# Kernel optimization log

Measured on AMD Instinct MI355X. Metric: run time of the kernel, lower is better.

## Reference

```python
import jax, jax.numpy as jnp
import numpy as np

S, T, B = 1024, 64, 8
KEY_DIM, QUERY_DIM, HIDDEN = 512, 512, 256


def setup_inputs() -> dict:
    key = jax.random.key(0)
    ks = jax.random.split(key, 8)
    inp = {
        "key": jax.random.normal(ks[0], (S, B, KEY_DIM), dtype=jnp.float32),
        "query": jax.random.normal(ks[1], (T, B, QUERY_DIM), dtype=jnp.float32),
        # torch nn.Linear params, stored as (in, out) for x @ W
        "Wk": jax.random.normal(ks[2], (KEY_DIM, HIDDEN), dtype=jnp.float32) * (1.0 / np.sqrt(KEY_DIM)),
        "bk": jax.random.normal(ks[3], (HIDDEN,), dtype=jnp.float32) * 0.01,
        "Wq": jax.random.normal(ks[4], (QUERY_DIM, HIDDEN), dtype=jnp.float32) * (1.0 / np.sqrt(QUERY_DIM)),
        "bq": jax.random.normal(ks[5], (HIDDEN,), dtype=jnp.float32) * 0.01,
        "v": jax.random.normal(ks[6], (HIDDEN,), dtype=jnp.float32),
    }
    return inp


def reference(key, query, Wk, bk, Wq, bq, v):
    # key: (S, B, Dk), query: (T, B, Dq)
    key_proj = key @ Wk + bk          # (S, B, H)
    query_proj = query @ Wq + bq      # (T, B, H)
    # broadcast add: (T,1,B,H) + (1,S,B,H) -> (T,S,B,H)
    energy = jnp.tanh(query_proj[:, None, :, :] + key_proj[None, :, :, :])
    scores = jnp.einsum('tsbh,h->tsb', energy, v)  # (T, S, B)
    attn = jax.nn.softmax(scores, axis=1)          # softmax over key positions S
    return jnp.transpose(attn, (2, 0, 1))          # (B, T, S)
```

## Files before the change

kernel.cpp:

```cpp
#include <hip/hip_runtime.h>

#define S_DIM 1024
#define T_DIM 64
#define B_DIM 8
#define K_DIM 512
#define H_DIM 256

typedef _Float16 f16;
typedef __attribute__((ext_vector_type(4))) _Float16 f16x4;
typedef __attribute__((ext_vector_type(8))) _Float16 f16x8;
typedef __attribute__((ext_vector_type(4))) float f32x4;

__device__ __forceinline__ float fast_rcp(float x) { return __builtin_amdgcn_rcpf(x); }

__device__ __forceinline__ void gload16(const void* g, void* l) {
    __builtin_amdgcn_global_load_lds(
        (const __attribute__((address_space(1))) unsigned int*)g,
        (__attribute__((address_space(3))) unsigned int*)l, 16, 0, 0);
}

__global__ __launch_bounds__(256) void wconv_kernel(
    const float* __restrict__ Wk, const float* __restrict__ Wq,
    f16* __restrict__ WTk, f16* __restrict__ WTq)
{
    __shared__ float tile[64][65];
    const int idx = blockIdx.x;
    const float* W = (idx & 32) ? Wq : Wk;
    f16* WT = (idx & 32) ? WTq : WTk;
    const int t32 = idx & 31;
    const int k0 = (t32 >> 2) * 64, n0 = (t32 & 3) * 64;
    const int c = threadIdx.x & 63, r0 = threadIdx.x >> 6;
#pragma unroll
    for (int i = 0; i < 16; ++i) {
        int r = r0 + i * 4;
        tile[r][c] = W[(size_t)(k0 + r) * H_DIM + n0 + c];
    }
    __syncthreads();
#pragma unroll
    for (int i = 0; i < 16; ++i) {
        int r = r0 + i * 4;
        WT[(size_t)(n0 + r) * K_DIM + k0 + c] = (f16)tile[c][r];
    }
}

__global__ __launch_bounds__(256, 4) void proj_gemm_all(
    const float* __restrict__ key, const f16* __restrict__ WTk,
    const float* __restrict__ bk, float* __restrict__ ktT,
    const float* __restrict__ query, const f16* __restrict__ WTq,
    const float* __restrict__ bq, float* __restrict__ tq2)
{
    __shared__ __align__(16) char smem[2][16384];
    const int tid = threadIdx.x;
    const int lane = tid & 63, wid = tid >> 6;
    const int widu = __builtin_amdgcn_readfirstlane(wid);
    const int wm = (wid >> 1) * 16, wn = (wid & 1) * 32;

    const int bid0 = blockIdx.x;
    const int bid = (bid0 & 7) * 136 + (bid0 >> 3);
    const bool isQ = bid >= 1024;
    const int lb = isQ ? bid - 1024 : bid;
    const size_t m0 = (size_t)(lb >> 2) * 32;
    const int n0 = (lb & 3) * 64;
    const float* A    = isQ ? query : key;
    const f16* BT     = isQ ? WTq : WTk;
    const float* bias = isQ ? bq : bk;

    const int o0 = tid << 4;
    const int o1 = o0 + 4096;
    const int row0 = o0 >> 7, kb0 = (o0 & 127) ^ ((row0 & 7) << 4);
    const int row1 = o1 >> 7, kb1 = (o1 & 127) ^ ((row1 & 7) << 4);
    const char* b_t = (const char*)(BT + (size_t)n0 * K_DIM);

    auto GLOADB = [&](int buf, int t) {
        const int kb = t * 128;
        char* d0 = &smem[buf][8192 + widu * 1024];
        gload16(b_t + (size_t)row0 * 1024 + kb + kb0, d0);
        gload16(b_t + (size_t)row1 * 1024 + kb + kb1, d0 + 4096);
    };

    const float* a_base = A + m0 * K_DIM;
    float4 areg[2];
    auto ALOAD = [&](int t) {
#pragma unroll
        for (int j = 0; j < 2; ++j) {
            const int fidx = j * 256 + tid;
            const int r = fidx >> 4, c16 = fidx & 15;
            areg[j] = *(const float4*)&a_base[(size_t)r * K_DIM + t * 64 + c16 * 4];
        }
    };
    auto AWRITE = [&](int buf) {
#pragma unroll
        for (int j = 0; j < 2; ++j) {
            const int fidx = j * 256 + tid;
            const int r = fidx >> 4, c16 = fidx & 15;
            const int byt = r * 128 + ((c16 * 8) ^ ((r & 7) << 4));
            f16 h0 = (f16)areg[j].x, h1 = (f16)areg[j].y, h2 = (f16)areg[j].z, h3 = (f16)areg[j].w;
            f16x4 hi = {h0, h1, h2, h3};
            f16x4 lo = {(f16)(areg[j].x - (float)h0), (f16)(areg[j].y - (float)h1),
                        (f16)(areg[j].z - (float)h2), (f16)(areg[j].w - (float)h3)};
            *(f16x4*)&smem[buf][byt] = hi;
            *(f16x4*)&smem[buf][4096 + byt] = lo;
        }
    };

    f32x4 acc[2] = {};
    const int fr = lane & 15, fgb = (lane >> 4) << 4;

    auto COMPUTE = [&](int buf) {
#pragma unroll
        for (int kk = 0; kk < 2; ++kk) {
            const int kbyte = kk * 64 + fgb;
            const int arow = wm + fr;
            const int abyt = (arow << 7) + (kbyte ^ ((arow & 7) << 4));
            f16x8 ah = *(const f16x8*)&smem[buf][abyt];
            f16x8 al = *(const f16x8*)&smem[buf][4096 + abyt];
            const int brow0 = wn + fr, brow1 = wn + 16 + fr;
            f16x8 b0 = *(const f16x8*)&smem[buf][8192 + (brow0 << 7) + (kbyte ^ ((brow0 & 7) << 4))];
            f16x8 b1 = *(const f16x8*)&smem[buf][8192 + (brow1 << 7) + (kbyte ^ ((brow1 & 7) << 4))];
            acc[0] = __builtin_amdgcn_mfma_f32_16x16x32_f16(ah, b0, acc[0], 0, 0, 0);
            acc[1] = __builtin_amdgcn_mfma_f32_16x16x32_f16(ah, b1, acc[1], 0, 0, 0);
            acc[0] = __builtin_amdgcn_mfma_f32_16x16x32_f16(al, b0, acc[0], 0, 0, 0);
            acc[1] = __builtin_amdgcn_mfma_f32_16x16x32_f16(al, b1, acc[1], 0, 0, 0);
        }
    };

    ALOAD(0);
    GLOADB(0, 0);
    AWRITE(0);
    __syncthreads();

    int buf = 0;
#pragma unroll 1
    for (int t = 0; t < 8; ++t) {
        if (t < 7) {
            ALOAD(t + 1);
            GLOADB(buf ^ 1, t + 1);
        }
        COMPUTE(buf);
        if (t < 7) {
            AWRITE(buf ^ 1);
            __syncthreads();
        }
        buf ^= 1;
    }

    const int crow = (lane >> 4) * 4, ccol = lane & 15;
    if (isQ) {
#pragma unroll
        for (int g = 0; g < 2; ++g) {
            int col = n0 + wn + g * 16 + ccol;
            float bv = bias[col];
#pragma unroll
            for (int r = 0; r < 4; ++r) {
                size_t row = m0 + wm + crow + r;
                float val = __expf(2.0f * (acc[g][r] + bv));
                tq2[((size_t)(row & 7) * T_DIM + (row >> 3)) * H_DIM + col] = val;
            }
        }
    } else {
        float* lt = (float*)&smem[0][0];
#pragma unroll
        for (int g = 0; g < 2; ++g) {
            int lcol = wn + g * 16 + ccol;
            float bv = bias[n0 + lcol];
#pragma unroll
            for (int r = 0; r < 4; ++r) {
                int lrow = wm + crow + r;
                lt[lrow * 64 + lcol] = __expf(2.0f * (acc[g][r] + bv));
            }
        }
        __syncthreads();
        const int sbase = (int)(m0 >> 3);
        const int n0q = n0 >> 2;
#pragma unroll
        for (int p = 0; p < 2; ++p) {
            int c = p * 256 + tid;
            int s_off = c & 3, h4 = (c >> 2) & 15, b2 = c >> 6;
            float4 o = *(const float4*)&lt[(s_off * 8 + b2) * 64 + h4 * 4];
            size_t f4idx = ((size_t)b2 * 64 + n0q + h4) * S_DIM + sbase + s_off;
            *(float4*)&ktT[f4idx * 4] = o;
        }
    }
}

__global__ __launch_bounds__(1024) void scores_softmax_kernel(
    const float* __restrict__ ktT, const float* __restrict__ tq2,
    const float* __restrict__ v, float* __restrict__ out)
{
    __shared__ float redm[2][16], reds[2][16];
    const int tid = threadIdx.x, lane = tid & 63;
    const int wid = __builtin_amdgcn_readfirstlane(tid >> 6);
    const int bid = blockIdx.x;
    const int b = bid & 7;
    const int t0 = (bid >> 3) * 2;
    const int s = tid;

    const float4* kb4 = (const float4*)ktT + (size_t)b * 64 * S_DIM + s;
    const float* q0p = tq2 + ((size_t)b * T_DIM + t0) * H_DIM;
    const float* q1p = q0p + H_DIM;

    float a0 = 0.f, a1 = 0.f;
#pragma unroll 8
    for (int h4 = 0; h4 < H_DIM / 4; ++h4) {
        float4 k4 = kb4[(size_t)h4 * S_DIM];
        float4 vv = *(const float4*)&v[h4 * 4];
        float4 q0 = *(const float4*)&q0p[h4 * 4];
        float4 q1 = *(const float4*)&q1p[h4 * 4];
        float A, B;
        A = fmaf(q0.x, k4.x, 1.0f); B = fmaf(q0.y, k4.y, 1.0f);
        a0 = fmaf(fmaf(vv.x, B, vv.y * A), fast_rcp(A * B), a0);
        A = fmaf(q0.z, k4.z, 1.0f); B = fmaf(q0.w, k4.w, 1.0f);
        a0 = fmaf(fmaf(vv.z, B, vv.w * A), fast_rcp(A * B), a0);
        A = fmaf(q1.x, k4.x, 1.0f); B = fmaf(q1.y, k4.y, 1.0f);
        a1 = fmaf(fmaf(vv.x, B, vv.y * A), fast_rcp(A * B), a1);
        A = fmaf(q1.z, k4.z, 1.0f); B = fmaf(q1.w, k4.w, 1.0f);
        a1 = fmaf(fmaf(vv.z, B, vv.w * A), fast_rcp(A * B), a1);
    }
    a0 *= -2.0f;
    a1 *= -2.0f;

    float m0 = a0, m1 = a1;
#pragma unroll
    for (int mm = 32; mm >= 1; mm >>= 1) {
        m0 = fmaxf(m0, __shfl_xor(m0, mm, 64));
        m1 = fmaxf(m1, __shfl_xor(m1, mm, 64));
    }
    if (lane == 0) { redm[0][wid] = m0; redm[1][wid] = m1; }
    __syncthreads();
    m0 = redm[0][0]; m1 = redm[1][0];
#pragma unroll
    for (int i = 1; i < 16; ++i) {
        m0 = fmaxf(m0, redm[0][i]);
        m1 = fmaxf(m1, redm[1][i]);
    }

    float e0 = __expf(a0 - m0), e1 = __expf(a1 - m1);
    float s0 = e0, s1 = e1;
#pragma unroll
    for (int mm = 32; mm >= 1; mm >>= 1) {
        s0 += __shfl_xor(s0, mm, 64);
        s1 += __shfl_xor(s1, mm, 64);
    }
    if (lane == 0) { reds[0][wid] = s0; reds[1][wid] = s1; }
    __syncthreads();
    s0 = 0.f; s1 = 0.f;
#pragma unroll
    for (int i = 0; i < 16; ++i) { s0 += reds[0][i]; s1 += reds[1][i]; }

    float* o = out + ((size_t)b * T_DIM + t0) * S_DIM + s;
    o[0]     = e0 * fast_rcp(s0);
    o[S_DIM] = e1 * fast_rcp(s1);
}

extern "C" void kernel_launch(void* const* d_in, const int* in_sizes, int n_in,
                              void* d_out, int out_size, void* d_ws, size_t ws_size,
                              hipStream_t stream)
{
    const float* key   = (const float*)d_in[0];
    const float* query = (const float*)d_in[1];
    const float* Wk    = (const float*)d_in[2];
    const float* bk    = (const float*)d_in[3];
    const float* Wq    = (const float*)d_in[4];
    const float* bq    = (const float*)d_in[5];
    const float* v     = (const float*)d_in[6];
    float* out = (float*)d_out;

    float* ktT    = (float*)d_ws;
    float* tq2    = ktT + (size_t)B_DIM * H_DIM * S_DIM;
    f16* WTk = (f16*)(tq2 + (size_t)B_DIM * T_DIM * H_DIM);
    f16* WTq = WTk + (size_t)H_DIM * K_DIM;

    wconv_kernel<<<64, 256, 0, stream>>>(Wk, Wq, WTk, WTq);
    proj_gemm_all<<<1088, 256, 0, stream>>>(key, WTk, bk, ktT, query, WTq, bq, tq2);
    scores_softmax_kernel<<<256, 1024, 0, stream>>>(ktT, tq2, v, out);
}
```

Before: 44.13 us.

## Double projection GEMM M-tile to 64 rows, halving block count

The projection GEMM tile grows from 32x64 to 64x64 per block. Each wave now computes a 32x32 sub-tile with four accumulators, so every B-fragment load from LDS feeds twice as many MFMAs. The grid shrinks from 1088 to 544 blocks and the launch bound drops to 3 blocks per CU. The LDS staging for the ktT transpose is re-laid out with a padded stride of 68. The cost is more registers and LDS per block and fewer blocks to spread across CUs, which may reduce latency hiding.

New measurement: 43.09 us. 2.4% less time.

```diff
diff --git a/kernel.cpp b/kernel.cpp
--- a/kernel.cpp
+++ b/kernel.cpp
@@ -43,29 +43,29 @@
     }
 }
 
-__global__ __launch_bounds__(256, 4) void proj_gemm_all(
+__global__ __launch_bounds__(256, 3) void proj_gemm_all(
     const float* __restrict__ key, const f16* __restrict__ WTk,
     const float* __restrict__ bk, float* __restrict__ ktT,
     const float* __restrict__ query, const f16* __restrict__ WTq,
     const float* __restrict__ bq, float* __restrict__ tq2)
 {
-    __shared__ __align__(16) char smem[2][16384];
+    __shared__ __align__(16) char smem[2][3][8192];
     const int tid = threadIdx.x;
     const int lane = tid & 63, wid = tid >> 6;
     const int widu = __builtin_amdgcn_readfirstlane(wid);
-    const int wm = (wid >> 1) * 16, wn = (wid & 1) * 32;
+    const int wm = (wid >> 1) * 32, wn = (wid & 1) * 32;
 
     const int bid0 = blockIdx.x;
-    const int bid = (bid0 & 7) * 136 + (bid0 >> 3);
-    const bool isQ = bid >= 1024;
-    const int lb = isQ ? bid - 1024 : bid;
-    const size_t m0 = (size_t)(lb >> 2) * 32;
+    const int bid = (bid0 & 7) * 68 + (bid0 >> 3);
+    const bool isQ = bid >= 512;
+    const int lb = isQ ? bid - 512 : bid;
+    const size_t m0 = (size_t)(lb >> 2) * 64;
     const int n0 = (lb & 3) * 64;
     const float* A    = isQ ? query : key;
     const f16* BT     = isQ ? WTq : WTk;
     const float* bias = isQ ? bq : bk;
 
-    const int o0 = tid << 4;
+    const int o0 = wid * 1024 + (lane << 4);
     const int o1 = o0 + 4096;
     const int row0 = o0 >> 7, kb0 = (o0 & 127) ^ ((row0 & 7) << 4);
     const int row1 = o1 >> 7, kb1 = (o1 & 127) ^ ((row1 & 7) << 4);
@@ -73,16 +73,16 @@
 
     auto GLOADB = [&](int buf, int t) {
         const int kb = t * 128;
-        char* d0 = &smem[buf][8192 + widu * 1024];
+        char* d0 = &smem[buf][2][widu * 1024];
         gload16(b_t + (size_t)row0 * 1024 + kb + kb0, d0);
         gload16(b_t + (size_t)row1 * 1024 + kb + kb1, d0 + 4096);
     };
 
     const float* a_base = A + m0 * K_DIM;
-    float4 areg[2];
+    float4 areg[4];
     auto ALOAD = [&](int t) {
 #pragma unroll
-        for (int j = 0; j < 2; ++j) {
+        for (int j = 0; j < 4; ++j) {
             const int fidx = j * 256 + tid;
             const int r = fidx >> 4, c16 = fidx & 15;
             areg[j] = *(const float4*)&a_base[(size_t)r * K_DIM + t * 64 + c16 * 4];
@@ -90,7 +90,7 @@
     };
     auto AWRITE = [&](int buf) {
 #pragma unroll
-        for (int j = 0; j < 2; ++j) {
+        for (int j = 0; j < 4; ++j) {
             const int fidx = j * 256 + tid;
             const int r = fidx >> 4, c16 = fidx & 15;
             const int byt = r * 128 + ((c16 * 8) ^ ((r & 7) << 4));
@@ -98,29 +98,33 @@
             f16x4 hi = {h0, h1, h2, h3};
             f16x4 lo = {(f16)(areg[j].x - (float)h0), (f16)(areg[j].y - (float)h1),
                         (f16)(areg[j].z - (float)h2), (f16)(areg[j].w - (float)h3)};
-            *(f16x4*)&smem[buf][byt] = hi;
-            *(f16x4*)&smem[buf][4096 + byt] = lo;
-        }
-    };
-
-    f32x4 acc[2] = {};
+            *(f16x4*)&smem[buf][0][byt] = hi;
+            *(f16x4*)&smem[buf][1][byt] = lo;
+        }
+    };
+
+    f32x4 acc[2][2] = {};
     const int fr = lane & 15, fgb = (lane >> 4) << 4;
 
     auto COMPUTE = [&](int buf) {
 #pragma unroll
         for (int kk = 0; kk < 2; ++kk) {
             const int kbyte = kk * 64 + fgb;
-            const int arow = wm + fr;
-            const int abyt = (arow << 7) + (kbyte ^ ((arow & 7) << 4));
-            f16x8 ah = *(const f16x8*)&smem[buf][abyt];
-            f16x8 al = *(const f16x8*)&smem[buf][4096 + abyt];
-            const int brow0 = wn + fr, brow1 = wn + 16 + fr;
-            f16x8 b0 = *(const f16x8*)&smem[buf][8192 + (brow0 << 7) + (kbyte ^ ((brow0 & 7) << 4))];
-            f16x8 b1 = *(const f16x8*)&smem[buf][8192 + (brow1 << 7) + (kbyte ^ ((brow1 & 7) << 4))];
-            acc[0] = __builtin_amdgcn_mfma_f32_16x16x32_f16(ah, b0, acc[0], 0, 0, 0);
-            acc[1] = __builtin_amdgcn_mfma_f32_16x16x32_f16(ah, b1, acc[1], 0, 0, 0);
-            acc[0] = __builtin_amdgcn_mfma_f32_16x16x32_f16(al, b0, acc[0], 0, 0, 0);
-            acc[1] = __builtin_amdgcn_mfma_f32_16x16x32_f16(al, b1, acc[1], 0, 0, 0);
+            auto ld = [&](int arr, int row) -> f16x8 {
+                int byt = ((row << 7) + kbyte) ^ ((row & 7) << 4);
+                return *(const f16x8*)&smem[buf][arr][byt];
+            };
+            f16x8 ah0 = ld(0, wm + fr),      ah1 = ld(0, wm + 16 + fr);
+            f16x8 al0 = ld(1, wm + fr),      al1 = ld(1, wm + 16 + fr);
+            f16x8 b0  = ld(2, wn + fr),      b1  = ld(2, wn + 16 + fr);
+            acc[0][0] = __builtin_amdgcn_mfma_f32_16x16x32_f16(ah0, b0, acc[0][0], 0, 0, 0);
+            acc[0][1] = __builtin_amdgcn_mfma_f32_16x16x32_f16(ah0, b1, acc[0][1], 0, 0, 0);
+            acc[1][0] = __builtin_amdgcn_mfma_f32_16x16x32_f16(ah1, b0, acc[1][0], 0, 0, 0);
+            acc[1][1] = __builtin_amdgcn_mfma_f32_16x16x32_f16(ah1, b1, acc[1][1], 0, 0, 0);
+            acc[0][0] = __builtin_amdgcn_mfma_f32_16x16x32_f16(al0, b0, acc[0][0], 0, 0, 0);
+            acc[0][1] = __builtin_amdgcn_mfma_f32_16x16x32_f16(al0, b1, acc[0][1], 0, 0, 0);
+            acc[1][0] = __builtin_amdgcn_mfma_f32_16x16x32_f16(al1, b0, acc[1][0], 0, 0, 0);
+            acc[1][1] = __builtin_amdgcn_mfma_f32_16x16x32_f16(al1, b1, acc[1][1], 0, 0, 0);
         }
     };
 
@@ -132,51 +136,49 @@
     int buf = 0;
 #pragma unroll 1
     for (int t = 0; t < 8; ++t) {
-        if (t < 7) {
-            ALOAD(t + 1);
-            GLOADB(buf ^ 1, t + 1);
-        }
+        if (t < 7) { ALOAD(t + 1); GLOADB(buf ^ 1, t + 1); }
         COMPUTE(buf);
-        if (t < 7) {
-            AWRITE(buf ^ 1);
-            __syncthreads();
-        }
+        if (t < 7) { AWRITE(buf ^ 1); __syncthreads(); }
         buf ^= 1;
     }
 
     const int crow = (lane >> 4) * 4, ccol = lane & 15;
     if (isQ) {
 #pragma unroll
-        for (int g = 0; g < 2; ++g) {
-            int col = n0 + wn + g * 16 + ccol;
-            float bv = bias[col];
-#pragma unroll
-            for (int r = 0; r < 4; ++r) {
-                size_t row = m0 + wm + crow + r;
-                float val = __expf(2.0f * (acc[g][r] + bv));
-                tq2[((size_t)(row & 7) * T_DIM + (row >> 3)) * H_DIM + col] = val;
+        for (int f = 0; f < 2; ++f)
+#pragma unroll
+            for (int g = 0; g < 2; ++g) {
+                int col = n0 + wn + g * 16 + ccol;
+                float bv = bias[col];
+#pragma unroll
+                for (int r = 0; r < 4; ++r) {
+                    size_t row = m0 + wm + f * 16 + crow + r;
+                    float val = __expf(2.0f * (acc[f][g][r] + bv));
+                    tq2[((size_t)(row & 7) * T_DIM + (row >> 3)) * H_DIM + col] = val;
+                }
             }
-        }
     } else {
-        float* lt = (float*)&smem[0][0];
-#pragma unroll
-        for (int g = 0; g < 2; ++g) {
-            int lcol = wn + g * 16 + ccol;
-            float bv = bias[n0 + lcol];
-#pragma unroll
-            for (int r = 0; r < 4; ++r) {
-                int lrow = wm + crow + r;
-                lt[lrow * 64 + lcol] = __expf(2.0f * (acc[g][r] + bv));
+        float* lt = (float*)&smem[0][0][0];
+#pragma unroll
+        for (int f = 0; f < 2; ++f)
+#pragma unroll
+            for (int g = 0; g < 2; ++g) {
+                int lcol = wn + g * 16 + ccol;
+                float bv = bias[n0 + lcol];
+#pragma unroll
+                for (int r = 0; r < 4; ++r) {
+                    int rr = wm + f * 16 + crow + r;
+                    lt[((rr & 7) * 8 + (rr >> 3)) * 68 + lcol] = __expf(2.0f * (acc[f][g][r] + bv));
+                }
             }
-        }
         __syncthreads();
         const int sbase = (int)(m0 >> 3);
         const int n0q = n0 >> 2;
 #pragma unroll
-        for (int p = 0; p < 2; ++p) {
+        for (int p = 0; p < 4; ++p) {
             int c = p * 256 + tid;
-            int s_off = c & 3, h4 = (c >> 2) & 15, b2 = c >> 6;
-            float4 o = *(const float4*)&lt[(s_off * 8 + b2) * 64 + h4 * 4];
+            int s_off = c & 7, h4 = (c >> 3) & 15, b2 = c >> 7;
+            float4 o = *(const float4*)&lt[(b2 * 8 + s_off) * 68 + h4 * 4];
             size_t f4idx = ((size_t)b2 * 64 + n0q + h4) * S_DIM + sbase + s_off;
             *(float4*)&ktT[f4idx * 4] = o;
         }
@@ -271,6 +273,6 @@
     f16* WTq = WTk + (size_t)H_DIM * K_DIM;
 
     wconv_kernel<<<64, 256, 0, stream>>>(Wk, Wq, WTk, WTq);
-    proj_gemm_all<<<1088, 256, 0, stream>>>(key, WTk, bk, ktT, query, WTq, bq, tq2);
+    proj_gemm_all<<<544, 256, 0, stream>>>(key, WTk, bk, ktT, query, WTq, bq, tq2);
     scores_softmax_kernel<<<256, 1024, 0, stream>>>(ktT, tq2, v, out);
 }
```
